# Kernel tuning notes

Measured on AMD Instinct MI355X. Metric: run time of the kernel, lower is better.

The kernel has to match this reference:

```python
import jax, jax.numpy as jnp
import numpy as np

N_NODES = 100000
N_EDGES = 1000000
DE = 128  # edge_embed_size
DN = 128  # node_embed_size


def _seg_mean(E, dst, num_nodes):
    # DGL mean reducer: nodes with no incoming edges get 0
    s = jax.ops.segment_sum(E, dst, num_segments=num_nodes)          # [N, de]
    c = jax.ops.segment_sum(jnp.ones((E.shape[0],), E.dtype), dst,
                            num_segments=num_nodes)                  # [N]
    return s / jnp.maximum(c, 1.0)[:, None]


def setup_inputs() -> dict:
    key = jax.random.key(0)
    ks = jax.random.split(key, 9)
    E_C = jax.random.normal(ks[0], (N_EDGES, DE), dtype=jnp.float32)
    E_D = jax.random.normal(ks[1], (N_EDGES, DE), dtype=jnp.float32)
    E_M = jax.random.normal(ks[2], (N_EDGES, DE), dtype=jnp.float32)
    dst_C = jax.random.randint(ks[3], (N_EDGES,), 0, N_NODES, dtype=jnp.int32)
    dst_D = jax.random.randint(ks[4], (N_EDGES,), 0, N_NODES, dtype=jnp.int32)
    dst_M = jax.random.randint(ks[5], (N_EDGES,), 0, N_NODES, dtype=jnp.int32)
    # Linear weights (no bias), stored so that y = x @ W
    W1 = jax.random.normal(ks[6], (DE, DE), dtype=jnp.float32) / np.sqrt(DE)
    W2 = jax.random.normal(ks[7], (DE, 1), dtype=jnp.float32) / np.sqrt(DE)
    W3 = jax.random.normal(ks[8], (DE, DN), dtype=jnp.float32) / np.sqrt(DE)
    return {"E_C": E_C, "E_D": E_D, "E_M": E_M,
            "dst_C": dst_C, "dst_D": dst_D, "dst_M": dst_M,
            "num_nodes": N_NODES, "W1": W1, "W2": W2, "W3": W3}


def reference(E_C, E_D, E_M, dst_C, dst_D, dst_M, num_nodes, W1, W2, W3):
    # per-relation copy_e + mean reduction to destination nodes
    YC = _seg_mean(E_C, dst_C, num_nodes)  # [N, de]
    YD = _seg_mean(E_D, dst_D, num_nodes)
    YM = _seg_mean(E_M, dst_M, num_nodes)
    Y = jnp.stack((YC, YD, YM), axis=1)    # [N, 3, de]
    # tanh-gated attention scores per relation: fc2(tanh(fc1(Y)))
    e = jnp.einsum('nrd,do->nro', jnp.tanh(jnp.einsum('nrd,de->nre', Y, W1)), W2)  # [N,3,1]
    a = jax.nn.softmax(e[..., 0], axis=1)[..., None]  # [N,3,1]
    OY = jnp.sum(a * Y, axis=1)            # [N, de]
    return OY @ W3                          # [N, dn]
```

## Files before the change

### kernel.cpp

```cpp
#include <hip/hip_runtime.h>
#include <hip/hip_bf16.h>
#include <hip/hip_fp16.h>

#define DE 128
#define NPB 16
#define CAP 64

typedef float f4 __attribute__((ext_vector_type(4)));
typedef int   i4 __attribute__((ext_vector_type(4)));

__global__ __launch_bounds__(256) void fill_direct4(
        const int* __restrict__ d0, const int* __restrict__ d1,
        const int* __restrict__ d2, int* __restrict__ cnt,
        int* __restrict__ eid, int N, int n0, int n1, int n2) {
    const int r = blockIdx.y;
    const int nr = (r == 0) ? n0 : (r == 1) ? n1 : n2;
    const int* d = (r == 0) ? d0 : (r == 1) ? d1 : d2;
    const int base = (r == 0) ? 0 : (r == 1) ? n0 : n0 + n1;
    int* cnt_r = cnt + (size_t)r * N;

    int i = (blockIdx.x * 256 + threadIdx.x) * 4;
    if (i >= nr) return;
    if (i + 4 <= nr) {
        i4 nd = *reinterpret_cast<const i4*>(d + i);
        #pragma unroll
        for (int u = 0; u < 4; ++u) {
            int node = nd[u];
            int p = atomicAdd(&cnt_r[node], 1);
            if (p < CAP) eid[(((size_t)r * N + node) << 6) + p] = i + u;
        }
    } else {
        for (int u = 0; i + u < nr; ++u) {
            int node = d[i + u];
            int p = atomicAdd(&cnt_r[node], 1);
            if (p < CAP) eid[(((size_t)r * N + node) << 6) + p] = i + u;
        }
    }
}

__global__ __launch_bounds__(256, 8) void node_fused(
        const float* __restrict__ E0, const float* __restrict__ E1,
        const float* __restrict__ E2,
        const int* __restrict__ eid,
        const int* __restrict__ cnt,
        const float* __restrict__ W1, const float* __restrict__ W2,
        const float* __restrict__ W3,
        float* __restrict__ out, int N) {
    const int g = threadIdx.x >> 5;
    const int t = threadIdx.x & 31;
    const int ln0 = g * 2;
    const int ln1 = ln0 + 1;

    __shared__ __half Ysh[NPB][3][DE];

    const float* Es[3] = { E0, E1, E2 };

    #pragma unroll 1
    for (int n2 = 0; n2 < 2; ++n2) {
        const int ln = ln0 + n2;
        int node = blockIdx.x * NPB + ln;
        if (node >= N) node = N - 1;

        #pragma unroll
        for (int r = 0; r < 3; ++r) {
            size_t slot = (size_t)r * N + node;
            int deg = cnt[slot];
            const int* el = eid + (slot << 6);
            const float* E = Es[r];
            f4 acc = {0.f, 0.f, 0.f, 0.f};

            int k = 0;
            for (; k + 8 <= deg; k += 8) {
                i4 ea = *reinterpret_cast<const i4*>(el + k);
                i4 eb = *reinterpret_cast<const i4*>(el + k + 4);
                f4 v0 = __builtin_nontemporal_load(reinterpret_cast<const f4*>(E + (size_t)ea[0] * DE + t * 4));
                f4 v1 = __builtin_nontemporal_load(reinterpret_cast<const f4*>(E + (size_t)ea[1] * DE + t * 4));
                f4 v2 = __builtin_nontemporal_load(reinterpret_cast<const f4*>(E + (size_t)ea[2] * DE + t * 4));
                f4 v3 = __builtin_nontemporal_load(reinterpret_cast<const f4*>(E + (size_t)ea[3] * DE + t * 4));
                f4 v4 = __builtin_nontemporal_load(reinterpret_cast<const f4*>(E + (size_t)eb[0] * DE + t * 4));
                f4 v5 = __builtin_nontemporal_load(reinterpret_cast<const f4*>(E + (size_t)eb[1] * DE + t * 4));
                f4 v6 = __builtin_nontemporal_load(reinterpret_cast<const f4*>(E + (size_t)eb[2] * DE + t * 4));
                f4 v7 = __builtin_nontemporal_load(reinterpret_cast<const f4*>(E + (size_t)eb[3] * DE + t * 4));
                acc += ((v0 + v1) + (v2 + v3)) + ((v4 + v5) + (v6 + v7));
            }
            if (k + 4 <= deg) {
                i4 ea = *reinterpret_cast<const i4*>(el + k);
                f4 v0 = __builtin_nontemporal_load(reinterpret_cast<const f4*>(E + (size_t)ea[0] * DE + t * 4));
                f4 v1 = __builtin_nontemporal_load(reinterpret_cast<const f4*>(E + (size_t)ea[1] * DE + t * 4));
                f4 v2 = __builtin_nontemporal_load(reinterpret_cast<const f4*>(E + (size_t)ea[2] * DE + t * 4));
                f4 v3 = __builtin_nontemporal_load(reinterpret_cast<const f4*>(E + (size_t)ea[3] * DE + t * 4));
                acc += (v0 + v1) + (v2 + v3);
                k += 4;
            }
            for (; k < deg; ++k) {
                int e = el[k];
                f4 v = __builtin_nontemporal_load(reinterpret_cast<const f4*>(E + (size_t)e * DE + t * 4));
                acc += v;
            }

            float inv = 1.0f / fmaxf((float)deg, 1.0f);
            acc *= inv;
            __half2 h0 = __floats2half2_rn(acc[0], acc[1]);
            __half2 h1 = __floats2half2_rn(acc[2], acc[3]);
            *reinterpret_cast<__half2*>(&Ysh[ln][r][t * 4])     = h0;
            *reinterpret_cast<__half2*>(&Ysh[ln][r][t * 4 + 2]) = h1;
        }
    }

    f4 z0 = {0,0,0,0}, z1 = {0,0,0,0}, z2 = {0,0,0,0};
    f4 z3 = {0,0,0,0}, z4 = {0,0,0,0}, z5 = {0,0,0,0};
    {
        const float* w1p = W1 + t * 4;
        #pragma unroll 2
        for (int d = 0; d < DE; d += 2) {
            f4 wA = *reinterpret_cast<const f4*>(w1p + (size_t)d * DE);
            f4 wB = *reinterpret_cast<const f4*>(w1p + (size_t)(d + 1) * DE);
            float2 a0 = __half22float2(*reinterpret_cast<const __half2*>(&Ysh[ln0][0][d]));
            float2 a1 = __half22float2(*reinterpret_cast<const __half2*>(&Ysh[ln0][1][d]));
            float2 a2 = __half22float2(*reinterpret_cast<const __half2*>(&Ysh[ln0][2][d]));
            float2 b0 = __half22float2(*reinterpret_cast<const __half2*>(&Ysh[ln1][0][d]));
            float2 b1 = __half22float2(*reinterpret_cast<const __half2*>(&Ysh[ln1][1][d]));
            float2 b2 = __half22float2(*reinterpret_cast<const __half2*>(&Ysh[ln1][2][d]));
            z0 += a0.x * wA + a0.y * wB;
            z1 += a1.x * wA + a1.y * wB;
            z2 += a2.x * wA + a2.y * wB;
            z3 += b0.x * wA + b0.y * wB;
            z4 += b1.x * wA + b1.y * wB;
            z5 += b2.x * wA + b2.y * wB;
        }
    }

    f4 w2v = *reinterpret_cast<const f4*>(W2 + t * 4);
    float s0 = 0.f, s1 = 0.f, s2 = 0.f, s3 = 0.f, s4 = 0.f, s5 = 0.f;
    #pragma unroll
    for (int j = 0; j < 4; ++j) {
        s0 = fmaf(tanhf(z0[j]), w2v[j], s0);
        s1 = fmaf(tanhf(z1[j]), w2v[j], s1);
        s2 = fmaf(tanhf(z2[j]), w2v[j], s2);
        s3 = fmaf(tanhf(z3[j]), w2v[j], s3);
        s4 = fmaf(tanhf(z4[j]), w2v[j], s4);
        s5 = fmaf(tanhf(z5[j]), w2v[j], s5);
    }
    #pragma unroll
    for (int m = 16; m >= 1; m >>= 1) {
        s0 += __shfl_xor(s0, m); s1 += __shfl_xor(s1, m); s2 += __shfl_xor(s2, m);
        s3 += __shfl_xor(s3, m); s4 += __shfl_xor(s4, m); s5 += __shfl_xor(s5, m);
    }

    {
        float mx = fmaxf(s0, fmaxf(s1, s2));
        float x0 = __expf(s0 - mx), x1 = __expf(s1 - mx), x2 = __expf(s2 - mx);
        float inv = 1.0f / (x0 + x1 + x2);
        float2 y0 = __half22float2(*reinterpret_cast<const __half2*>(&Ysh[ln0][0][t * 4]));
        float2 y0b = __half22float2(*reinterpret_cast<const __half2*>(&Ysh[ln0][0][t * 4 + 2]));
        float2 y1 = __half22float2(*reinterpret_cast<const __half2*>(&Ysh[ln0][1][t * 4]));
        float2 y1b = __half22float2(*reinterpret_cast<const __half2*>(&Ysh[ln0][1][t * 4 + 2]));
        float2 y2 = __half22float2(*reinterpret_cast<const __half2*>(&Ysh[ln0][2][t * 4]));
        float2 y2b = __half22float2(*reinterpret_cast<const __half2*>(&Ysh[ln0][2][t * 4 + 2]));
        float c0 = x0 * inv, c1 = x1 * inv, c2 = x2 * inv;
        float o0 = c0 * y0.x + c1 * y1.x + c2 * y2.x;
        float o1 = c0 * y0.y + c1 * y1.y + c2 * y2.y;
        float o2 = c0 * y0b.x + c1 * y1b.x + c2 * y2b.x;
        float o3 = c0 * y0b.y + c1 * y1b.y + c2 * y2b.y;
        *reinterpret_cast<__half2*>(&Ysh[ln0][0][t * 4])     = __floats2half2_rn(o0, o1);
        *reinterpret_cast<__half2*>(&Ysh[ln0][0][t * 4 + 2]) = __floats2half2_rn(o2, o3);
    }
    {
        float mx = fmaxf(s3, fmaxf(s4, s5));
        float x0 = __expf(s3 - mx), x1 = __expf(s4 - mx), x2 = __expf(s5 - mx);
        float inv = 1.0f / (x0 + x1 + x2);
        float2 y0 = __half22float2(*reinterpret_cast<const __half2*>(&Ysh[ln1][0][t * 4]));
        float2 y0b = __half22float2(*reinterpret_cast<const __half2*>(&Ysh[ln1][0][t * 4 + 2]));
        float2 y1 = __half22float2(*reinterpret_cast<const __half2*>(&Ysh[ln1][1][t * 4]));
        float2 y1b = __half22float2(*reinterpret_cast<const __half2*>(&Ysh[ln1][1][t * 4 + 2]));
        float2 y2 = __half22float2(*reinterpret_cast<const __half2*>(&Ysh[ln1][2][t * 4]));
        float2 y2b = __half22float2(*reinterpret_cast<const __half2*>(&Ysh[ln1][2][t * 4 + 2]));
        float c0 = x0 * inv, c1 = x1 * inv, c2 = x2 * inv;
        float o0 = c0 * y0.x + c1 * y1.x + c2 * y2.x;
        float o1 = c0 * y0.y + c1 * y1.y + c2 * y2.y;
        float o2 = c0 * y0b.x + c1 * y1b.x + c2 * y2b.x;
        float o3 = c0 * y0b.y + c1 * y1b.y + c2 * y2b.y;
        *reinterpret_cast<__half2*>(&Ysh[ln1][0][t * 4])     = __floats2half2_rn(o0, o1);
        *reinterpret_cast<__half2*>(&Ysh[ln1][0][t * 4 + 2]) = __floats2half2_rn(o2, o3);
    }

    f4 o0 = {0,0,0,0}, o1 = {0,0,0,0};
    {
        const float* w3p = W3 + t * 4;
        #pragma unroll 2
        for (int d = 0; d < DE; d += 2) {
            f4 wA = *reinterpret_cast<const f4*>(w3p + (size_t)d * DE);
            f4 wB = *reinterpret_cast<const f4*>(w3p + (size_t)(d + 1) * DE);
            float2 a = __half22float2(*reinterpret_cast<const __half2*>(&Ysh[ln0][0][d]));
            float2 b = __half22float2(*reinterpret_cast<const __half2*>(&Ysh[ln1][0][d]));
            o0 += a.x * wA + a.y * wB;
            o1 += b.x * wA + b.y * wB;
        }
    }
    {
        int node0 = blockIdx.x * NPB + ln0;
        int node1 = node0 + 1;
        if (node0 < N)
            *reinterpret_cast<f4*>(out + (size_t)node0 * DE + t * 4) = o0;
        if (node1 < N)
            *reinterpret_cast<f4*>(out + (size_t)node1 * DE + t * 4) = o1;
    }
}

extern "C" void kernel_launch(void* const* d_in, const int* in_sizes, int n_in,
                              void* d_out, int out_size, void* d_ws, size_t ws_size,
                              hipStream_t stream) {
    const float* E_C = (const float*)d_in[0];
    const float* E_D = (const float*)d_in[1];
    const float* E_M = (const float*)d_in[2];
    const int* dst_C = (const int*)d_in[3];
    const int* dst_D = (const int*)d_in[4];
    const int* dst_M = (const int*)d_in[5];
    const float* W1 = (const float*)d_in[7];
    const float* W2 = (const float*)d_in[8];
    const float* W3 = (const float*)d_in[9];
    float* out = (float*)d_out;

    const int N = out_size / DE;
    const int nE[3] = { in_sizes[3], in_sizes[4], in_sizes[5] };
    const int nEmax = max(nE[0], max(nE[1], nE[2]));

    int* eid = (int*)d_ws;
    int* cnt = eid + (size_t)3 * N * CAP;

    (void)hipMemsetAsync(cnt, 0, 3 * (size_t)N * sizeof(int), stream);

    {
        dim3 grid((nEmax + 1023) / 1024, 3);
        fill_direct4<<<grid, 256, 0, stream>>>(dst_C, dst_D, dst_M, cnt, eid,
                                               N, nE[0], nE[1], nE[2]);
    }

    int nblocks = (N + NPB - 1) / NPB;
    node_fused<<<nblocks, 256, 0, stream>>>(
        E_C, E_D, E_M, eid, cnt, W1, W2, W3, out, N);
}
```

Measured before the change: 734.8 us.

## Use MFMA fp16 matrix cores for fc1 and output projection with swizzled LDS

Replaces the per-thread scalar FMA loops for the W1 and W3 matmuls with 16x16x32 fp16 MFMA instructions operating on a block of 16 nodes x 3 relations held in a swizzled shared-memory tile. A small prep kernel transposes and converts W1/W3 to fp16 in workspace each call. Attention score reduction now goes through a shared partial buffer with extra block barriers. This targets the compute portion after the gather, while the gather itself is unchanged and likely still dominant; it adds fp16 weight rounding and lowers the occupancy hint.

```diff
diff --git a/kernel.cpp b/kernel.cpp
--- a/kernel.cpp
+++ b/kernel.cpp
@@ -6,8 +6,13 @@
 #define NPB 16
 #define CAP 64
 
-typedef float f4 __attribute__((ext_vector_type(4)));
-typedef int   i4 __attribute__((ext_vector_type(4)));
+typedef float    f4 __attribute__((ext_vector_type(4)));
+typedef int      i4 __attribute__((ext_vector_type(4)));
+typedef _Float16 h8 __attribute__((ext_vector_type(8)));
+
+__device__ __forceinline__ int swz(int row, int col) {
+    return row * DE + (col ^ ((row & 7) << 3));
+}
 
 __global__ __launch_bounds__(256) void fill_direct4(
         const int* __restrict__ d0, const int* __restrict__ d1,
@@ -16,7 +21,6 @@
     const int r = blockIdx.y;
     const int nr = (r == 0) ? n0 : (r == 1) ? n1 : n2;
     const int* d = (r == 0) ? d0 : (r == 1) ? d1 : d2;
-    const int base = (r == 0) ? 0 : (r == 1) ? n0 : n0 + n1;
     int* cnt_r = cnt + (size_t)r * N;
 
     int i = (blockIdx.x * 256 + threadIdx.x) * 4;
@@ -38,172 +42,189 @@
     }
 }
 
-__global__ __launch_bounds__(256, 8) void node_fused(
+__global__ void prep_w(const float* __restrict__ W1, const float* __restrict__ W3,
+                       __half* __restrict__ W1T, __half* __restrict__ W3T) {
+    int i = blockIdx.x * 256 + threadIdx.x;
+    if (i < DE * DE) {
+        int n = i >> 7, k = i & 127;
+        W1T[i] = __float2half(W1[(size_t)k * DE + n]);
+        W3T[i] = __float2half(W3[(size_t)k * DE + n]);
+    }
+}
+
+__global__ __launch_bounds__(256, 6) void node_fused(
         const float* __restrict__ E0, const float* __restrict__ E1,
         const float* __restrict__ E2,
         const int* __restrict__ eid,
         const int* __restrict__ cnt,
-        const float* __restrict__ W1, const float* __restrict__ W2,
-        const float* __restrict__ W3,
+        const __half* __restrict__ W1T,
+        const float* __restrict__ W2,
+        const __half* __restrict__ W3T,
         float* __restrict__ out, int N) {
-    const int g = threadIdx.x >> 5;
-    const int t = threadIdx.x & 31;
-    const int ln0 = g * 2;
-    const int ln1 = ln0 + 1;
-
-    __shared__ __half Ysh[NPB][3][DE];
+    const int tid = threadIdx.x;
+
+    __shared__ __half Ysh[48 * DE];
+    __shared__ float e_part[4][48];
 
     const float* Es[3] = { E0, E1, E2 };
 
-    #pragma unroll 1
-    for (int n2 = 0; n2 < 2; ++n2) {
-        const int ln = ln0 + n2;
-        int node = blockIdx.x * NPB + ln;
-        if (node >= N) node = N - 1;
-
-        #pragma unroll
-        for (int r = 0; r < 3; ++r) {
-            size_t slot = (size_t)r * N + node;
-            int deg = cnt[slot];
-            const int* el = eid + (slot << 6);
-            const float* E = Es[r];
-            f4 acc = {0.f, 0.f, 0.f, 0.f};
-
-            int k = 0;
-            for (; k + 8 <= deg; k += 8) {
-                i4 ea = *reinterpret_cast<const i4*>(el + k);
-                i4 eb = *reinterpret_cast<const i4*>(el + k + 4);
-                f4 v0 = __builtin_nontemporal_load(reinterpret_cast<const f4*>(E + (size_t)ea[0] * DE + t * 4));
-                f4 v1 = __builtin_nontemporal_load(reinterpret_cast<const f4*>(E + (size_t)ea[1] * DE + t * 4));
-                f4 v2 = __builtin_nontemporal_load(reinterpret_cast<const f4*>(E + (size_t)ea[2] * DE + t * 4));
-                f4 v3 = __builtin_nontemporal_load(reinterpret_cast<const f4*>(E + (size_t)ea[3] * DE + t * 4));
-                f4 v4 = __builtin_nontemporal_load(reinterpret_cast<const f4*>(E + (size_t)eb[0] * DE + t * 4));
-                f4 v5 = __builtin_nontemporal_load(reinterpret_cast<const f4*>(E + (size_t)eb[1] * DE + t * 4));
-                f4 v6 = __builtin_nontemporal_load(reinterpret_cast<const f4*>(E + (size_t)eb[2] * DE + t * 4));
-                f4 v7 = __builtin_nontemporal_load(reinterpret_cast<const f4*>(E + (size_t)eb[3] * DE + t * 4));
-                acc += ((v0 + v1) + (v2 + v3)) + ((v4 + v5) + (v6 + v7));
-            }
-            if (k + 4 <= deg) {
-                i4 ea = *reinterpret_cast<const i4*>(el + k);
-                f4 v0 = __builtin_nontemporal_load(reinterpret_cast<const f4*>(E + (size_t)ea[0] * DE + t * 4));
-                f4 v1 = __builtin_nontemporal_load(reinterpret_cast<const f4*>(E + (size_t)ea[1] * DE + t * 4));
-                f4 v2 = __builtin_nontemporal_load(reinterpret_cast<const f4*>(E + (size_t)ea[2] * DE + t * 4));
-                f4 v3 = __builtin_nontemporal_load(reinterpret_cast<const f4*>(E + (size_t)ea[3] * DE + t * 4));
-                acc += (v0 + v1) + (v2 + v3);
-                k += 4;
-            }
-            for (; k < deg; ++k) {
-                int e = el[k];
-                f4 v = __builtin_nontemporal_load(reinterpret_cast<const f4*>(E + (size_t)e * DE + t * 4));
-                acc += v;
-            }
-
-            float inv = 1.0f / fmaxf((float)deg, 1.0f);
-            acc *= inv;
-            __half2 h0 = __floats2half2_rn(acc[0], acc[1]);
-            __half2 h1 = __floats2half2_rn(acc[2], acc[3]);
-            *reinterpret_cast<__half2*>(&Ysh[ln][r][t * 4])     = h0;
-            *reinterpret_cast<__half2*>(&Ysh[ln][r][t * 4 + 2]) = h1;
-        }
-    }
-
-    f4 z0 = {0,0,0,0}, z1 = {0,0,0,0}, z2 = {0,0,0,0};
-    f4 z3 = {0,0,0,0}, z4 = {0,0,0,0}, z5 = {0,0,0,0};
-    {
-        const float* w1p = W1 + t * 4;
-        #pragma unroll 2
-        for (int d = 0; d < DE; d += 2) {
-            f4 wA = *reinterpret_cast<const f4*>(w1p + (size_t)d * DE);
-            f4 wB = *reinterpret_cast<const f4*>(w1p + (size_t)(d + 1) * DE);
-            float2 a0 = __half22float2(*reinterpret_cast<const __half2*>(&Ysh[ln0][0][d]));
-            float2 a1 = __half22float2(*reinterpret_cast<const __half2*>(&Ysh[ln0][1][d]));
-            float2 a2 = __half22float2(*reinterpret_cast<const __half2*>(&Ysh[ln0][2][d]));
-            float2 b0 = __half22float2(*reinterpret_cast<const __half2*>(&Ysh[ln1][0][d]));
-            float2 b1 = __half22float2(*reinterpret_cast<const __half2*>(&Ysh[ln1][1][d]));
-            float2 b2 = __half22float2(*reinterpret_cast<const __half2*>(&Ysh[ln1][2][d]));
-            z0 += a0.x * wA + a0.y * wB;
-            z1 += a1.x * wA + a1.y * wB;
-            z2 += a2.x * wA + a2.y * wB;
-            z3 += b0.x * wA + b0.y * wB;
-            z4 += b1.x * wA + b1.y * wB;
-            z5 += b2.x * wA + b2.y * wB;
-        }
-    }
-
-    f4 w2v = *reinterpret_cast<const f4*>(W2 + t * 4);
-    float s0 = 0.f, s1 = 0.f, s2 = 0.f, s3 = 0.f, s4 = 0.f, s5 = 0.f;
+    {
+        const int g = tid >> 5;
+        const int t = tid & 31;
+        #pragma unroll 1
+        for (int n2 = 0; n2 < 2; ++n2) {
+            const int ln = g * 2 + n2;
+            int node = blockIdx.x * NPB + ln;
+            if (node >= N) node = N - 1;
+
+            #pragma unroll
+            for (int r = 0; r < 3; ++r) {
+                size_t slot = (size_t)r * N + node;
+                int deg = cnt[slot];
+                const int* el = eid + (slot << 6);
+                const float* E = Es[r];
+                f4 acc = {0.f, 0.f, 0.f, 0.f};
+
+                int k = 0;
+                for (; k + 8 <= deg; k += 8) {
+                    i4 ea = *reinterpret_cast<const i4*>(el + k);
+                    i4 eb = *reinterpret_cast<const i4*>(el + k + 4);
+                    f4 v0 = __builtin_nontemporal_load(reinterpret_cast<const f4*>(E + (size_t)ea[0] * DE + t * 4));
+                    f4 v1 = __builtin_nontemporal_load(reinterpret_cast<const f4*>(E + (size_t)ea[1] * DE + t * 4));
+                    f4 v2 = __builtin_nontemporal_load(reinterpret_cast<const f4*>(E + (size_t)ea[2] * DE + t * 4));
+                    f4 v3 = __builtin_nontemporal_load(reinterpret_cast<const f4*>(E + (size_t)ea[3] * DE + t * 4));
+                    f4 v4 = __builtin_nontemporal_load(reinterpret_cast<const f4*>(E + (size_t)eb[0] * DE + t * 4));
+                    f4 v5 = __builtin_nontemporal_load(reinterpret_cast<const f4*>(E + (size_t)eb[1] * DE + t * 4));
+                    f4 v6 = __builtin_nontemporal_load(reinterpret_cast<const f4*>(E + (size_t)eb[2] * DE + t * 4));
+                    f4 v7 = __builtin_nontemporal_load(reinterpret_cast<const f4*>(E + (size_t)eb[3] * DE + t * 4));
+                    acc += ((v0 + v1) + (v2 + v3)) + ((v4 + v5) + (v6 + v7));
+                }
+                if (k + 4 <= deg) {
+                    i4 ea = *reinterpret_cast<const i4*>(el + k);
+                    f4 v0 = __builtin_nontemporal_load(reinterpret_cast<const f4*>(E + (size_t)ea[0] * DE + t * 4));
+                    f4 v1 = __builtin_nontemporal_load(reinterpret_cast<const f4*>(E + (size_t)ea[1] * DE + t * 4));
+                    f4 v2 = __builtin_nontemporal_load(reinterpret_cast<const f4*>(E + (size_t)ea[2] * DE + t * 4));
+                    f4 v3 = __builtin_nontemporal_load(reinterpret_cast<const f4*>(E + (size_t)ea[3] * DE + t * 4));
+                    acc += (v0 + v1) + (v2 + v3);
+                    k += 4;
+                }
+                for (; k < deg; ++k) {
+                    int e = el[k];
+                    f4 v = __builtin_nontemporal_load(reinterpret_cast<const f4*>(E + (size_t)e * DE + t * 4));
+                    acc += v;
+                }
+
+                acc *= 1.0f / fmaxf((float)deg, 1.0f);
+                int row = r * 16 + ln;
+                int idx = swz(row, t * 4);
+                *reinterpret_cast<__half2*>(&Ysh[idx])     = __floats2half2_rn(acc[0], acc[1]);
+                *reinterpret_cast<__half2*>(&Ysh[idx + 2]) = __floats2half2_rn(acc[2], acc[3]);
+            }
+        }
+    }
+    __syncthreads();
+
+    const int l  = tid & 63;
+    const int w  = tid >> 6;
+    const int lo = l & 15;
+    const int hi = l >> 4;
+
+    f4 z00 = {0,0,0,0}, z01 = {0,0,0,0};
+    f4 z10 = {0,0,0,0}, z11 = {0,0,0,0};
+    f4 z20 = {0,0,0,0}, z21 = {0,0,0,0};
     #pragma unroll
-    for (int j = 0; j < 4; ++j) {
-        s0 = fmaf(tanhf(z0[j]), w2v[j], s0);
-        s1 = fmaf(tanhf(z1[j]), w2v[j], s1);
-        s2 = fmaf(tanhf(z2[j]), w2v[j], s2);
-        s3 = fmaf(tanhf(z3[j]), w2v[j], s3);
-        s4 = fmaf(tanhf(z4[j]), w2v[j], s4);
-        s5 = fmaf(tanhf(z5[j]), w2v[j], s5);
-    }
-    #pragma unroll
-    for (int m = 16; m >= 1; m >>= 1) {
-        s0 += __shfl_xor(s0, m); s1 += __shfl_xor(s1, m); s2 += __shfl_xor(s2, m);
-        s3 += __shfl_xor(s3, m); s4 += __shfl_xor(s4, m); s5 += __shfl_xor(s5, m);
-    }
-
-    {
-        float mx = fmaxf(s0, fmaxf(s1, s2));
-        float x0 = __expf(s0 - mx), x1 = __expf(s1 - mx), x2 = __expf(s2 - mx);
+    for (int kt = 0; kt < 4; ++kt) {
+        int kc = kt * 32 + hi * 8;
+        h8 a0 = *reinterpret_cast<const h8*>(&Ysh[swz(lo,      kc)]);
+        h8 a1 = *reinterpret_cast<const h8*>(&Ysh[swz(16 + lo, kc)]);
+        h8 a2 = *reinterpret_cast<const h8*>(&Ysh[swz(32 + lo, kc)]);
+        h8 b0 = *reinterpret_cast<const h8*>(&W1T[(size_t)(w * 32 + lo) * DE + kc]);
+        h8 b1 = *reinterpret_cast<const h8*>(&W1T[(size_t)(w * 32 + 16 + lo) * DE + kc]);
+        z00 = __builtin_amdgcn_mfma_f32_16x16x32_f16(a0, b0, z00, 0, 0, 0);
+        z01 = __builtin_amdgcn_mfma_f32_16x16x32_f16(a0, b1, z01, 0, 0, 0);
+        z10 = __builtin_amdgcn_mfma_f32_16x16x32_f16(a1, b0, z10, 0, 0, 0);
+        z11 = __builtin_amdgcn_mfma_f32_16x16x32_f16(a1, b1, z11, 0, 0, 0);
+        z20 = __builtin_amdgcn_mfma_f32_16x16x32_f16(a2, b0, z20, 0, 0, 0);
+        z21 = __builtin_amdgcn_mfma_f32_16x16x32_f16(a2, b1, z21, 0, 0, 0);
+    }
+
+    {
+        float w2c0 = W2[w * 32 + lo];
+        float w2c1 = W2[w * 32 + 16 + lo];
+        float p0[4], p1[4], p2[4];
+        #pragma unroll
+        for (int reg = 0; reg < 4; ++reg) {
+            p0[reg] = tanhf(z00[reg]) * w2c0 + tanhf(z01[reg]) * w2c1;
+            p1[reg] = tanhf(z10[reg]) * w2c0 + tanhf(z11[reg]) * w2c1;
+            p2[reg] = tanhf(z20[reg]) * w2c0 + tanhf(z21[reg]) * w2c1;
+        }
+        #pragma unroll
+        for (int m = 1; m <= 8; m <<= 1) {
+            #pragma unroll
+            for (int reg = 0; reg < 4; ++reg) {
+                p0[reg] += __shfl_xor(p0[reg], m);
+                p1[reg] += __shfl_xor(p1[reg], m);
+                p2[reg] += __shfl_xor(p2[reg], m);
+            }
+        }
+        if (lo == 0) {
+            #pragma unroll
+            for (int reg = 0; reg < 4; ++reg) {
+                int row = hi * 4 + reg;
+                e_part[w][row]      = p0[reg];
+                e_part[w][16 + row] = p1[reg];
+                e_part[w][32 + row] = p2[reg];
+            }
+        }
+    }
+    __syncthreads();
+
+    {
+        int ln = tid >> 4;
+        int c0 = (tid & 15) * 8;
+        float e0 = 0.f, e1 = 0.f, e2 = 0.f;
+        #pragma unroll
+        for (int ww = 0; ww < 4; ++ww) {
+            e0 += e_part[ww][ln];
+            e1 += e_part[ww][16 + ln];
+            e2 += e_part[ww][32 + ln];
+        }
+        float mx = fmaxf(e0, fmaxf(e1, e2));
+        float x0 = __expf(e0 - mx), x1 = __expf(e1 - mx), x2 = __expf(e2 - mx);
         float inv = 1.0f / (x0 + x1 + x2);
-        float2 y0 = __half22float2(*reinterpret_cast<const __half2*>(&Ysh[ln0][0][t * 4]));
-        float2 y0b = __half22float2(*reinterpret_cast<const __half2*>(&Ysh[ln0][0][t * 4 + 2]));
-        float2 y1 = __half22float2(*reinterpret_cast<const __half2*>(&Ysh[ln0][1][t * 4]));
-        float2 y1b = __half22float2(*reinterpret_cast<const __half2*>(&Ysh[ln0][1][t * 4 + 2]));
-        float2 y2 = __half22float2(*reinterpret_cast<const __half2*>(&Ysh[ln0][2][t * 4]));
-        float2 y2b = __half22float2(*reinterpret_cast<const __half2*>(&Ysh[ln0][2][t * 4 + 2]));
-        float c0 = x0 * inv, c1 = x1 * inv, c2 = x2 * inv;
-        float o0 = c0 * y0.x + c1 * y1.x + c2 * y2.x;
-        float o1 = c0 * y0.y + c1 * y1.y + c2 * y2.y;
-        float o2 = c0 * y0b.x + c1 * y1b.x + c2 * y2b.x;
-        float o3 = c0 * y0b.y + c1 * y1b.y + c2 * y2b.y;
-        *reinterpret_cast<__half2*>(&Ysh[ln0][0][t * 4])     = __floats2half2_rn(o0, o1);
-        *reinterpret_cast<__half2*>(&Ysh[ln0][0][t * 4 + 2]) = __floats2half2_rn(o2, o3);
-    }
-    {
-        float mx = fmaxf(s3, fmaxf(s4, s5));
-        float x0 = __expf(s3 - mx), x1 = __expf(s4 - mx), x2 = __expf(s5 - mx);
-        float inv = 1.0f / (x0 + x1 + x2);
-        float2 y0 = __half22float2(*reinterpret_cast<const __half2*>(&Ysh[ln1][0][t * 4]));
-        float2 y0b = __half22float2(*reinterpret_cast<const __half2*>(&Ysh[ln1][0][t * 4 + 2]));
-        float2 y1 = __half22float2(*reinterpret_cast<const __half2*>(&Ysh[ln1][1][t * 4]));
-        float2 y1b = __half22float2(*reinterpret_cast<const __half2*>(&Ysh[ln1][1][t * 4 + 2]));
-        float2 y2 = __half22float2(*reinterpret_cast<const __half2*>(&Ysh[ln1][2][t * 4]));
-        float2 y2b = __half22float2(*reinterpret_cast<const __half2*>(&Ysh[ln1][2][t * 4 + 2]));
-        float c0 = x0 * inv, c1 = x1 * inv, c2 = x2 * inv;
-        float o0 = c0 * y0.x + c1 * y1.x + c2 * y2.x;
-        float o1 = c0 * y0.y + c1 * y1.y + c2 * y2.y;
-        float o2 = c0 * y0b.x + c1 * y1b.x + c2 * y2b.x;
-        float o3 = c0 * y0b.y + c1 * y1b.y + c2 * y2b.y;
-        *reinterpret_cast<__half2*>(&Ysh[ln1][0][t * 4])     = __floats2half2_rn(o0, o1);
-        *reinterpret_cast<__half2*>(&Ysh[ln1][0][t * 4 + 2]) = __floats2half2_rn(o2, o3);
-    }
-
-    f4 o0 = {0,0,0,0}, o1 = {0,0,0,0};
-    {
-        const float* w3p = W3 + t * 4;
-        #pragma unroll 2
-        for (int d = 0; d < DE; d += 2) {
-            f4 wA = *reinterpret_cast<const f4*>(w3p + (size_t)d * DE);
-            f4 wB = *reinterpret_cast<const f4*>(w3p + (size_t)(d + 1) * DE);
-            float2 a = __half22float2(*reinterpret_cast<const __half2*>(&Ysh[ln0][0][d]));
-            float2 b = __half22float2(*reinterpret_cast<const __half2*>(&Ysh[ln1][0][d]));
-            o0 += a.x * wA + a.y * wB;
-            o1 += b.x * wA + b.y * wB;
-        }
-    }
-    {
-        int node0 = blockIdx.x * NPB + ln0;
-        int node1 = node0 + 1;
-        if (node0 < N)
-            *reinterpret_cast<f4*>(out + (size_t)node0 * DE + t * 4) = o0;
-        if (node1 < N)
-            *reinterpret_cast<f4*>(out + (size_t)node1 * DE + t * 4) = o1;
+        float a0 = x0 * inv, a1 = x1 * inv, a2 = x2 * inv;
+
+        h8 y0 = *reinterpret_cast<const h8*>(&Ysh[swz(ln,      c0)]);
+        h8 y1 = *reinterpret_cast<const h8*>(&Ysh[swz(16 + ln, c0)]);
+        h8 y2 = *reinterpret_cast<const h8*>(&Ysh[swz(32 + ln, c0)]);
+        h8 o;
+        #pragma unroll
+        for (int j = 0; j < 8; ++j)
+            o[j] = (_Float16)(a0 * (float)y0[j] + a1 * (float)y1[j] + a2 * (float)y2[j]);
+        *reinterpret_cast<h8*>(&Ysh[swz(ln, c0)]) = o;
+    }
+    __syncthreads();
+
+    {
+        f4 o0 = {0,0,0,0}, o1 = {0,0,0,0};
+        #pragma unroll
+        for (int kt = 0; kt < 4; ++kt) {
+            int kc = kt * 32 + hi * 8;
+            h8 a  = *reinterpret_cast<const h8*>(&Ysh[swz(lo, kc)]);
+            h8 b0 = *reinterpret_cast<const h8*>(&W3T[(size_t)(w * 32 + lo) * DE + kc]);
+            h8 b1 = *reinterpret_cast<const h8*>(&W3T[(size_t)(w * 32 + 16 + lo) * DE + kc]);
+            o0 = __builtin_amdgcn_mfma_f32_16x16x32_f16(a, b0, o0, 0, 0, 0);
+            o1 = __builtin_amdgcn_mfma_f32_16x16x32_f16(a, b1, o1, 0, 0, 0);
+        }
+        int nodebase = blockIdx.x * NPB;
+        #pragma unroll
+        for (int reg = 0; reg < 4; ++reg) {
+            int node = nodebase + hi * 4 + reg;
+            if (node < N) {
+                out[(size_t)node * DE + w * 32 + lo]      = o0[reg];
+                out[(size_t)node * DE + w * 32 + 16 + lo] = o1[reg];
+            }
+        }
     }
 }
 
@@ -227,8 +248,11 @@
 
     int* eid = (int*)d_ws;
     int* cnt = eid + (size_t)3 * N * CAP;
+    __half* W1T = (__half*)(cnt + (size_t)3 * N);
+    __half* W3T = W1T + DE * DE;
 
     (void)hipMemsetAsync(cnt, 0, 3 * (size_t)N * sizeof(int), stream);
+    prep_w<<<(DE * DE + 255) / 256, 256, 0, stream>>>(W1, W3, W1T, W3T);
 
     {
         dim3 grid((nEmax + 1023) / 1024, 3);
@@ -238,5 +262,5 @@
 
     int nblocks = (N + NPB - 1) / NPB;
     node_fused<<<nblocks, 256, 0, stream>>>(
-        E_C, E_D, E_M, eid, cnt, W1, W2, W3, out, N);
-}
+        E_C, E_D, E_M, eid, cnt, W1T, W2, W3T, out, N);
+}
```

Result: faster. 593.8 us (-19.2%).
